# Kernel tuning notes

Measured on AMD Instinct MI355X. Metric: run time of the kernel, lower is better.

Reference implementation:

```python
import jax, jax.numpy as jnp
import numpy as np

B, S, E, O, LAYERS = 256, 28, 256, 256, 3


def setup_inputs() -> dict:
    key = jax.random.key(0)
    ks = jax.random.split(key, 20)
    sc = 0.05
    inp = {
        "centers": jax.random.normal(ks[0], (B, S, 3), jnp.float32),
        "object_embedding": jax.random.normal(ks[1], (B, S, E), jnp.float32),
        "counts": jax.random.randint(ks[2], (B,), 1, S + 1),
        # linear_relation_object: 3 -> E
        "Wr": jax.random.normal(ks[3], (E, 3), jnp.float32) * sc,
        "br": jnp.zeros((E,), jnp.float32),
        # LSTM (PyTorch gate order i,f,g,o)
        "W_ih": jax.random.normal(ks[4], (4 * O, E), jnp.float32) * sc,
        "W_hh": jax.random.normal(ks[5], (4 * O, O), jnp.float32) * sc,
        "b_ih": jnp.zeros((4 * O,), jnp.float32),
        "b_hh": jnp.zeros((4 * O,), jnp.float32),
        # gr: 3E -> O
        "Wgr": jax.random.normal(ks[6], (O, 3 * E), jnp.float32) * sc,
        "bgr": jnp.zeros((O,), jnp.float32),
        # bezier control: O -> O, plus scalar alpha
        "Wbc": jax.random.normal(ks[7], (O, O), jnp.float32) * sc,
        "bbc": jnp.zeros((O,), jnp.float32),
        "alpha": jnp.asarray(0.5, jnp.float32),
        # esa: E -> O
        "Wesa": jax.random.normal(ks[8], (O, E), jnp.float32) * sc,
        "besa": jnp.zeros((O,), jnp.float32),
        # gaussian heads: O -> 3
        "Wmu": jax.random.normal(ks[9], (3, O), jnp.float32) * sc,
        "bmu": jnp.zeros((3,), jnp.float32),
        "Wlv": jax.random.normal(ks[10], (3, O), jnp.float32) * sc,
        "blv": jnp.zeros((3,), jnp.float32),
    }
    return inp


def _lstm(x, W_ih, W_hh, b_ih, b_hh):
    # x: [B,S,E] -> hs: [B,S,O], zero initial state, PyTorch gate order i,f,g,o
    Bdim = x.shape[0]
    Odim = W_hh.shape[1]
    b = b_ih + b_hh

    def step(carry, xt):
        h, c = carry
        z = xt @ W_ih.T + h @ W_hh.T + b  # [B,4O]
        i, f, g, o = jnp.split(z, 4, axis=-1)
        c = jax.nn.sigmoid(f) * c + jax.nn.sigmoid(i) * jnp.tanh(g)
        h = jax.nn.sigmoid(o) * jnp.tanh(c)
        return (h, c), h

    h0 = jnp.zeros((Bdim, Odim), x.dtype)
    _, hs = jax.lax.scan(step, (h0, h0), jnp.swapaxes(x, 0, 1))
    return jnp.swapaxes(hs, 0, 1)


def reference(centers, object_embedding, counts, Wr, br, W_ih, W_hh, b_ih, b_hh,
              Wgr, bgr, Wbc, bbc, alpha, Wesa, besa, Wmu, bmu, Wlv, blv):
    # masks from per-scene object counts (padding replication of the torch loops)
    idx = jnp.arange(S)
    obj_mask = (idx[None, :] < counts[:, None]).astype(jnp.float32)[..., None]  # [B,S,1]
    rel_mask = (obj_mask[:, :, None, :] * obj_mask[:, None, :, :])              # [B,S,S,1]

    centers_p = centers * obj_mask                     # padded centers are zero
    relation = centers_p[:, :, None, :] - centers_p[:, None, :, :]  # [B,S,S,3]
    rlf = relation @ Wr.T + br                         # [B,S,S,E]

    olf = object_embedding * obj_mask                  # [B,S,E]
    t = jax.nn.sigmoid(alpha)

    for _ in range(LAYERS):
        new_olf = _lstm(olf, W_ih, W_hh, b_ih, b_hh) * obj_mask
        rep_i = jnp.broadcast_to(olf[:, :, None, :], (olf.shape[0], S, S, olf.shape[-1]))
        rep_j = jnp.broadcast_to(olf[:, None, :, :], (olf.shape[0], S, S, olf.shape[-1]))
        cat = jnp.concatenate([rep_i, rep_j, rlf], axis=-1)   # [B,S,S,3E]
        rlf_lin = cat @ Wgr.T + bgr                           # [B,S,S,O]
        cp = rlf_lin @ Wbc.T + bbc
        bez = ((1 - t) ** 2 + t ** 2) * rlf_lin + 2 * (1 - t) * t * cp
        rlf = jnp.tanh(bez) * rel_mask
        olf = new_olf

    rlf = rlf @ Wesa.T + besa                                  # [B,S,S,O]
    # base attention: softmax over dim=1 (explicit max-subtract as in source)
    base_attn = jax.nn.softmax(rlf - jnp.max(rlf, axis=1, keepdims=True), axis=1)
    # gaussian attention (eval mode: eps = 0 -> samples = mus)
    mus = rlf @ Wmu.T + bmu                                    # [B,S,S,3]
    _logvars = rlf @ Wlv.T + blv                               # computed, unused at eval
    gscores = jnp.mean(mus, axis=-1, keepdims=True)            # [B,S,S,1]
    gattn = jax.nn.softmax(gscores, axis=1)
    attn = 0.5 * base_attn + 0.5 * gattn                       # broadcast over O
    rel_out = jnp.sum(attn * rlf, axis=-2) * obj_mask          # [B,S,O]
    return rel_out
```

## Files before the change

### kernel.cpp

```cpp
#include <hip/hip_runtime.h>


typedef __attribute__((ext_vector_type(8))) short short8;
typedef __attribute__((ext_vector_type(4))) float f32x4;

__device__ __forceinline__ float b2f(unsigned short u){
  union { unsigned int i; float f; } v; v.i = ((unsigned int)u) << 16; return v.f;
}
__device__ __forceinline__ float u2f(unsigned int u){
  union { unsigned int i; float f; } v; v.i = u; return v.f;
}
__device__ __forceinline__ unsigned short f2b(float f){
  union { float f; unsigned int i; } v; v.f = f;
  return (unsigned short)((v.i + 0x8000u) >> 16);
}
__device__ __forceinline__ unsigned int pk2(float lo, float hi){
  union { float f; unsigned int i; } a, b; a.f = lo; b.f = hi;
  return __builtin_amdgcn_perm(b.i + 0x8000u, a.i + 0x8000u, 0x07060302u);
}
__device__ __forceinline__ float sigm(float x){ return 1.f/(1.f+__expf(-x)); }
__device__ __forceinline__ float tanh_f(float x){ float e = __expf(2.f*x); return 1.f - 2.f/(e+1.f); }
__device__ __forceinline__ int xsw(int row, int n){
  int c = n >> 3;
  int pc = (c & 24) | ((c ^ row) & 7);
  return row*256 + pc*8 + (n & 7);
}

#define MFMA16(a,b,c) __builtin_amdgcn_mfma_f32_16x16x32_bf16((a),(b),(c),0,0,0)

__global__ __launch_bounds__(256) void k_reprep(const float* __restrict__ Wih,
                                                const float* __restrict__ Whh,
                                                const float* __restrict__ Wgr,
                                                const float* __restrict__ Wbc,
                                                const float* __restrict__ Wesa,
                                                const float* __restrict__ Wmu,
                                                unsigned short* __restrict__ wcv,
                                                float* __restrict__ wmean,
                                                const float* __restrict__ emb,
                                                const int* __restrict__ counts,
                                                unsigned short* __restrict__ olf,
                                                float* __restrict__ out){
  if (blockIdx.x >= 3329){
    int bs = blockIdx.x - 3329;
    int b = bs / 28; int s = bs - b*28;
    int e = threadIdx.x;
    olf[(size_t)bs*256 + e] = (s < counts[b]) ? f2b(emb[(size_t)bs*256 + e]) : (unsigned short)0;
    out[(size_t)bs*256 + e] = 0.f;
    return;
  }
  int i = blockIdx.x*256 + threadIdx.x;
  if (i >= 851968){
    int o = i - 851968;
    if (o < 256) wmean[o] = (Wmu[o] + Wmu[256+o] + Wmu[512+o]) * (1.f/3.f);
    return;
  }
  const float* s; int segbase, N, stride, off, local;
  if      (i < 262144){ s=Wih;  segbase=0;      N=1024; stride=256; off=0;   local=i; }
  else if (i < 524288){ s=Whh;  segbase=262144; N=1024; stride=256; off=0;   local=i-262144; }
  else if (i < 589824){ s=Wgr;  segbase=524288; N=256;  stride=768; off=0;   local=i-524288; }
  else if (i < 655360){ s=Wgr;  segbase=589824; N=256;  stride=768; off=256; local=i-589824; }
  else if (i < 720896){ s=Wgr;  segbase=655360; N=256;  stride=768; off=512; local=i-655360; }
  else if (i < 786432){ s=Wbc;  segbase=720896; N=256;  stride=256; off=0;   local=i-720896; }
  else                { s=Wesa; segbase=786432; N=256;  stride=256; off=0;   local=i-786432; }
  int n = local >> 8, k = local & 255;
  wcv[segbase + (((k >> 3)*N + n) << 3) + (k & 7)] = f2b(s[n*stride + off + k]);
}

__global__ __launch_bounds__(256) void k_xgemm(const unsigned short* __restrict__ olf,
                                               const unsigned short* __restrict__ Wih,
                                               unsigned short* __restrict__ zx){
  const int tid = threadIdx.x;
  const int wid = tid >> 6, lane = tid & 63, col = lane & 15, quad = lane >> 4;
  const int m0 = (blockIdx.x >> 1)*64 + wid*16;
  const int nt0 = (blockIdx.x & 1)*32;
  short8 af[8];
  #pragma unroll
  for (int kt=0; kt<8; ++kt)
    af[kt] = *(const short8*)&olf[(size_t)(m0 + col)*256 + kt*32 + quad*8];
  #pragma unroll 4
  for (int nt=nt0; nt<nt0+32; ++nt){
    int n = nt*16 + col;
    f32x4 acc = (f32x4){0.f,0.f,0.f,0.f};
    #pragma unroll
    for (int kt=0; kt<8; ++kt){
      short8 bf = *(const short8*)&Wih[((((kt*4 + quad) << 10) + n) << 3)];
      acc = MFMA16(bf, af[kt], acc);
    }
    *(uint2*)&zx[(size_t)(m0 + col)*1024 + nt*16 + quad*4] =
        make_uint2(pk2(acc[0],acc[1]), pk2(acc[2],acc[3]));
  }
}

__global__ __launch_bounds__(1024) void k_recat(const unsigned short* __restrict__ zx,
                                                const unsigned short* __restrict__ Whh,
                                                const float* __restrict__ bih,
                                                const float* __restrict__ bhh,
                                                const int* __restrict__ counts,
                                                unsigned short* __restrict__ olf_out,
                                                const unsigned short* __restrict__ olf_at,
                                                const unsigned short* __restrict__ Wgri,
                                                const unsigned short* __restrict__ Wgrj,
                                                const float* __restrict__ bgr,
                                                unsigned short* __restrict__ At_out){
  __shared__ unsigned short Ab[2][16*264];
  const int tid = threadIdx.x;
  const int wv = tid >> 6, lane = tid & 63, col = lane & 15, quad = lane >> 4;

  if (blockIdx.x >= 16){
    const int m0 = (blockIdx.x - 16)*256 + wv*16;
    short8 af[8];
    #pragma unroll
    for (int kt=0; kt<8; ++kt)
      af[kt] = *(const short8*)&olf_at[(size_t)(m0 + col)*256 + kt*32 + quad*8];
    #pragma unroll 4
    for (int nt=0; nt<32; ++nt){
      const unsigned short* wb = (nt < 16) ? Wgri : Wgrj;
      int nb = (nt < 16) ? 0 : 256;
      int nn = (nt & 15)*16 + col;
      f32x4 bg4 = (nt < 16) ? *(const f32x4*)&bgr[(nt & 15)*16 + quad*4]
                            : (f32x4){0.f,0.f,0.f,0.f};
      f32x4 acc = (f32x4){0.f,0.f,0.f,0.f};
      #pragma unroll
      for (int kt=0; kt<8; ++kt){
        short8 bf = *(const short8*)&wb[((((kt*4 + quad) << 8) + nn) << 3)];
        acc = MFMA16(bf, af[kt], acc);
      }
      acc += bg4;
      *(uint2*)&At_out[(size_t)(m0 + col)*512 + nb + (nt & 15)*16 + quad*4] =
          make_uint2(pk2(acc[0],acc[1]), pk2(acc[2],acc[3]));
    }
    return;
  }
  const int sc0 = blockIdx.x * 16;
  const int u = wv*16 + col;
  float bz[4];
  #pragma unroll
  for (int g=0; g<4; ++g) bz[g] = bih[g*256+u] + bhh[g*256+u];
  int cnt4[4];
  #pragma unroll
  for (int r=0; r<4; ++r) cnt4[r] = counts[sc0 + quad*4 + r];

  float cst[4];
  #pragma unroll
  for (int r=0; r<4; ++r) cst[r] = 0.f;
  for (int i=tid; i<16*264; i+=1024) Ab[0][i] = 0;
  __syncthreads();

  for (int t=0; t<28; ++t){
    const int cur = t & 1, nxt = cur ^ 1;
    float zxv[4][4];
    #pragma unroll
    for (int g=0; g<4; ++g){
      #pragma unroll
      for (int r=0; r<4; ++r)
        zxv[g][r] = b2f(zx[((size_t)(sc0 + quad*4 + r)*28 + t)*1024 + g*256 + u]);
    }
    f32x4 acc[4];
    #pragma unroll
    for (int g=0; g<4; ++g) acc[g] = (f32x4){0.f,0.f,0.f,0.f};
    #pragma unroll
    for (int kt=0; kt<8; ++kt){
      short8 a = *(const short8*)&Ab[cur][col*264 + kt*32 + quad*8];
      #pragma unroll
      for (int g=0; g<4; ++g){
        short8 bf = *(const short8*)&Whh[((((kt*4 + quad) << 10) + g*256 + u) << 3)];
        acc[g] = MFMA16(a, bf, acc[g]);
      }
    }
    #pragma unroll
    for (int r=0; r<4; ++r){
      int s = quad*4 + r;
      float zi = acc[0][r] + zxv[0][r] + bz[0];
      float zf = acc[1][r] + zxv[1][r] + bz[1];
      float zg = acc[2][r] + zxv[2][r] + bz[2];
      float zo = acc[3][r] + zxv[3][r] + bz[3];
      float cc = sigm(zf)*cst[r] + sigm(zi)*tanh_f(zg);
      cst[r] = cc;
      float hh = sigm(zo)*tanh_f(cc);
      unsigned short hb = f2b(hh);
      Ab[nxt][s*264 + u] = hb;
      olf_out[((size_t)(sc0+s)*28 + t)*256 + u] = (t < cnt4[r]) ? hb : (unsigned short)0;
    }
    __syncthreads();
  }
}

__global__ __launch_bounds__(256) void k_aterm(const unsigned short* __restrict__ olf,
                                               const unsigned short* __restrict__ Wgri,
                                               const unsigned short* __restrict__ Wgrj,
                                               const float* __restrict__ bgr,
                                               unsigned short* __restrict__ Aout){
  const int tid = threadIdx.x;
  const int wid = tid >> 6, lane = tid & 63, col = lane & 15, quad = lane >> 4;
  const int m0 = blockIdx.x*64 + wid*16;
  short8 af[8];
  #pragma unroll
  for (int kt=0; kt<8; ++kt)
    af[kt] = *(const short8*)&olf[(size_t)(m0 + col)*256 + kt*32 + quad*8];
  #pragma unroll 4
  for (int nt=0; nt<32; ++nt){
    const unsigned short* wb = (nt < 16) ? Wgri : Wgrj;
    int nb = (nt < 16) ? 0 : 256;
    int nn = (nt & 15)*16 + col;
    f32x4 bg4 = (nt < 16) ? *(const f32x4*)&bgr[(nt & 15)*16 + quad*4]
                          : (f32x4){0.f,0.f,0.f,0.f};
    f32x4 acc = (f32x4){0.f,0.f,0.f,0.f};
    #pragma unroll
    for (int kt=0; kt<8; ++kt){
      short8 bf = *(const short8*)&wb[((((kt*4 + quad) << 8) + nn) << 3)];
      acc = MFMA16(bf, af[kt], acc);
    }
    acc += bg4;
    *(uint2*)&Aout[(size_t)(m0 + col)*512 + nb + (nt & 15)*16 + quad*4] =
        make_uint2(pk2(acc[0],acc[1]), pk2(acc[2],acc[3]));
  }
}

#define GEMM_TILE64(SRC, WPTR)                                                      \
  {                                                                                 \
    _Pragma("unroll")                                                               \
    for (int rf=0; rf<4; ++rf){ Ya[rf][0]=(f32x4){0.f,0.f,0.f,0.f};                 \
                                Ya[rf][1]=(f32x4){0.f,0.f,0.f,0.f}; }               \
    _Pragma("unroll 1")                                                             \
    for (int kc=0; kc<4; ++kc){                                                     \
      short8 av[2][4], bv[2][2];                                                    \
      _Pragma("unroll")                                                             \
      for (int u=0; u<2; ++u){                                                      \
        int kt = kc*2 + u;                                                          \
        _Pragma("unroll")                                                           \
        for (int rf=0; rf<4; ++rf)                                                  \
          av[u][rf] = *(const short8*)&(SRC)[(Abase[rf] + kc*64) ^ (u*32)];         \
        bv[u][0] = *(const short8*)&(WPTR)[Bbase + kt*8192];                        \
        bv[u][1] = *(const short8*)&(WPTR)[Bbase + kt*8192 + 128];                  \
      }                                                                             \
      __builtin_amdgcn_s_setprio(1);                                                \
      _Pragma("unroll")                                                             \
      for (int u=0; u<2; ++u){                                                      \
        _Pragma("unroll")                                                           \
        for (int rf=0; rf<4; ++rf){                                                 \
          Ya[rf][0] = MFMA16(bv[u][0], av[u][rf], Ya[rf][0]);                       \
          Ya[rf][1] = MFMA16(bv[u][1], av[u][rf], Ya[rf][1]);                       \
        }                                                                           \
      }                                                                             \
      __builtin_amdgcn_s_setprio(0);                                                \
    }                                                                               \
  }

__global__ __launch_bounds__(512, 4) void k_mega(
    const float* __restrict__ centers, const int* __restrict__ counts,
    const float* __restrict__ Wr, const float* __restrict__ br,
    const unsigned short* __restrict__ Wgrr, const float* __restrict__ bgr,
    const unsigned short* __restrict__ Wbc, const float* __restrict__ bbc,
    const float* __restrict__ alpha,
    const unsigned short* __restrict__ Wesa, const float* __restrict__ besa,
    const float* __restrict__ wmean, const float* __restrict__ bmu,
    const unsigned short* __restrict__ Aterm, float* __restrict__ out){
  __shared__ unsigned short Xa[64*256];
  __shared__ unsigned short Yb[64*256];
  float* hrSBp = (float*)&Xa[56*256];
  float* gsbp  = (float*)&Xa[60*256];
  float* hrSGp = (float*)&Xa[60*256+128];
  const int tid = threadIdx.x;
  const int wv = tid >> 6;
  const int lane = tid & 63, col = lane & 15, quad = lane >> 4;
  const int xcd = blockIdx.x & 7, idx = blockIdx.x >> 3;
  const int b = xcd*32 + idx/14, jt = idx - (idx/14)*14;
  const int cb = counts[b];
  const int nbase = wv*32;

  float av_ = alpha[0];
  float tv = sigm(av_);
  float c1 = (1.f-tv)*(1.f-tv) + tv*tv;
  float c2 = 2.f*tv*(1.f-tv);

  float pv[4];
  const unsigned short* apI[4];
  const unsigned short* apJ[4];
  #pragma unroll
  for (int mt=0; mt<4; ++mt){
    int m = mt*16 + col;
    int i = m >> 1;
    int pi = (i < 27) ? i : 27;
    int pj = jt*2 + (m & 1);
    pv[mt] = (m < 56 && i < cb && pj < cb) ? 1.f : 0.f;
    apI[mt] = Aterm + (size_t)(b*28 + pi)*512 + nbase + quad*4;
    apJ[mt] = Aterm + (size_t)(b*28 + pj)*512 + 256 + nbase + quad*4;
  }
  int Abase[4];
  #pragma unroll
  for (int rf=0; rf<4; ++rf){
    int row = rf*16 + col;
    Abase[rf] = row*256 + ((quad ^ (row & 3)) | (row & 4))*8;
  }
  const int Bbase = (quad*256 + nbase + col)*8;
  int woff[4][2];
  f32x4 cbb[2], bev[2];
  #pragma unroll
  for (int nt2=0; nt2<2; ++nt2){
    int n0 = nbase + nt2*16 + quad*4;
    cbb[nt2] = (*(const f32x4*)&bbc[n0]) * c2;
    bev[nt2] = *(const f32x4*)&besa[n0];
    #pragma unroll
    for (int mt=0; mt<4; ++mt)
      woff[mt][nt2] = xsw(mt*16 + col, n0);
  }

  {
    int m = tid >> 3, sub = tid & 7;
    int i = m >> 1, j = jt*2 + (m & 1);
    bool valid = (m < 56);
    float mi = (valid && i < cb) ? 1.f : 0.f;
    float mj = (valid && j < cb) ? 1.f : 0.f;
    float vm = valid ? 1.f : 0.f;
    const float* ci = centers + (b*28 + (valid ? i : 0))*3;
    const float* cj = centers + (b*28 + j)*3;
    float dx = mi*ci[0] - mj*cj[0];
    float dy = mi*ci[1] - mj*cj[1];
    float dz = mi*ci[2] - mj*cj[2];
    #pragma unroll
    for (int c8=0; c8<4; ++c8){
      int e0 = sub*32 + c8*8;
      f32x4 w0 = *(const f32x4*)&Wr[e0*3 +  0];
      f32x4 w1 = *(const f32x4*)&Wr[e0*3 +  4];
      f32x4 w2 = *(const f32x4*)&Wr[e0*3 +  8];
      f32x4 w3 = *(const f32x4*)&Wr[e0*3 + 12];
      f32x4 w4 = *(const f32x4*)&Wr[e0*3 + 16];
      f32x4 w5 = *(const f32x4*)&Wr[e0*3 + 20];
      f32x4 b0 = *(const f32x4*)&br[e0];
      f32x4 b1 = *(const f32x4*)&br[e0+4];
      b0 *= vm; b1 *= vm;
      float v0 = dx*w0[0] + dy*w0[1] + dz*w0[2] + b0[0];
      float v1 = dx*w0[3] + dy*w1[0] + dz*w1[1] + b0[1];
      float v2 = dx*w1[2] + dy*w1[3] + dz*w2[0] + b0[2];
      float v3 = dx*w2[1] + dy*w2[2] + dz*w2[3] + b0[3];
      float v4 = dx*w3[0] + dy*w3[1] + dz*w3[2] + b1[0];
      float v5 = dx*w3[3] + dy*w4[0] + dz*w4[1] + b1[1];
      float v6 = dx*w4[2] + dy*w4[3] + dz*w5[0] + b1[2];
      float v7 = dx*w5[1] + dy*w5[2] + dz*w5[3] + b1[3];
      uint4 pw;
      pw.x = pk2(v0,v1); pw.y = pk2(v2,v3); pw.z = pk2(v4,v5); pw.w = pk2(v6,v7);
      *(uint4*)&Xa[xsw(m, e0)] = pw;
    }
  }
  __syncthreads();

  f32x4 Ya[4][2];
  #pragma unroll 1
  for (int l=0; l<3; ++l){
    uint2 rAi[4][2], rAj[4][2];
    #pragma unroll
    for (int mt=0; mt<4; ++mt){
      rAi[mt][0] = *(const uint2*)&apI[mt][0];
      rAi[mt][1] = *(const uint2*)&apI[mt][16];
      rAj[mt][0] = *(const uint2*)&apJ[mt][0];
      rAj[mt][1] = *(const uint2*)&apJ[mt][16];
      apI[mt] += 7168*512; apJ[mt] += 7168*512;
    }
    GEMM_TILE64(Xa, Wgrr);
    #pragma unroll
    for (int nt2=0; nt2<2; ++nt2){
      #pragma unroll
      for (int mt=0; mt<4; ++mt){
        uint2 wi = rAi[mt][nt2], wj = rAj[mt][nt2];
        f32x4 ai, aj;
        ai[0] = u2f(wi.x << 16); ai[1] = u2f(wi.x & 0xffff0000u);
        ai[2] = u2f(wi.y << 16); ai[3] = u2f(wi.y & 0xffff0000u);
        aj[0] = u2f(wj.x << 16); aj[1] = u2f(wj.x & 0xffff0000u);
        aj[2] = u2f(wj.y << 16); aj[3] = u2f(wj.y & 0xffff0000u);
        f32x4 v = Ya[mt][nt2] + ai + aj;
        *(uint2*)&Yb[woff[mt][nt2]] = make_uint2(pk2(v[0],v[1]), pk2(v[2],v[3]));
      }
    }
    __syncthreads();
    GEMM_TILE64(Yb, Wbc);
    #pragma unroll
    for (int nt2=0; nt2<2; ++nt2){
      #pragma unroll
      for (int mt=0; mt<4; ++mt){
        uint2 w = *(const uint2*)&Yb[woff[mt][nt2]];
        f32x4 rl;
        rl[0] = u2f(w.x << 16); rl[1] = u2f(w.x & 0xffff0000u);
        rl[2] = u2f(w.y << 16); rl[3] = u2f(w.y & 0xffff0000u);
        f32x4 bez = Ya[mt][nt2]*c2 + cbb[nt2];
        bez = rl*c1 + bez;
        float x0 = tanh_f(bez[0]) * pv[mt];
        float x1 = tanh_f(bez[1]) * pv[mt];
        float x2 = tanh_f(bez[2]) * pv[mt];
        float x3 = tanh_f(bez[3]) * pv[mt];
        *(uint2*)&Xa[woff[mt][nt2]] = make_uint2(pk2(x0,x1), pk2(x2,x3));
      }
    }
    __syncthreads();
  }
  GEMM_TILE64(Xa, Wesa);
  __syncthreads();
  f32x4 sbp[2] = {(f32x4){0.f,0.f,0.f,0.f}, (f32x4){0.f,0.f,0.f,0.f}};
  const float m3f = (col < 8) ? 1.f : 0.f;
  #pragma unroll
  for (int nt2=0; nt2<2; ++nt2){
    #pragma unroll
    for (int mt=0; mt<4; ++mt){
      f32x4 v = Ya[mt][nt2] + bev[nt2];
      *(uint2*)&Yb[woff[mt][nt2]] = make_uint2(pk2(v[0],v[1]), pk2(v[2],v[3]));
      f32x4 e;
      e[0] = __expf(v[0]); e[1] = __expf(v[1]);
      e[2] = __expf(v[2]); e[3] = __expf(v[3]);
      *(uint2*)&Xa[woff[mt][nt2]] = make_uint2(pk2(e[0],e[1]), pk2(e[2],e[3]));
      f32x4 wsum = e;
      if (mt == 3) wsum *= m3f;
      sbp[nt2] += wsum;
    }
  }
  f32x4 hr[2];
  #pragma unroll
  for (int nt2=0; nt2<2; ++nt2){
    #pragma unroll
    for (int r=0; r<4; ++r){
      float s = sbp[nt2][r];
      s += __shfl_xor(s, 2, 64);
      s += __shfl_xor(s, 4, 64);
      s += __shfl_xor(s, 8, 64);
      hr[nt2][r] = 0.5f / s;
    }
  }
  __syncthreads();
  {
    int m = tid >> 3, sub = tid & 7;
    if (m < 56){
      float s = 0.f;
      #pragma unroll
      for (int c8=0; c8<4; ++c8){
        int e0 = sub*32 + c8*8;
        uint4 u = *(const uint4*)&Yb[xsw(m, e0)];
        f32x4 wm0 = *(const f32x4*)&wmean[e0];
        f32x4 wm1 = *(const f32x4*)&wmean[e0+4];
        s += u2f(u.x << 16)*wm0[0] + u2f(u.x & 0xffff0000u)*wm0[1]
           + u2f(u.y << 16)*wm0[2] + u2f(u.y & 0xffff0000u)*wm0[3]
           + u2f(u.z << 16)*wm1[0] + u2f(u.z & 0xffff0000u)*wm1[1]
           + u2f(u.w << 16)*wm1[2] + u2f(u.w & 0xffff0000u)*wm1[3];
      }
      s += __shfl_xor(s, 1, 64);
      s += __shfl_xor(s, 2, 64);
      s += __shfl_xor(s, 4, 64);
      if (sub == 0)
        gsbp[m] = __expf(s + (bmu[0] + bmu[1] + bmu[2])*(1.f/3.f));
    }
  }
  if (col < 2){
    #pragma unroll
    for (int nt2=0; nt2<2; ++nt2){
      #pragma unroll
      for (int r=0; r<4; ++r)
        hrSBp[col*256 + nbase + nt2*16 + quad*4 + r] = hr[nt2][r];
    }
  }
  __syncthreads();
  if (tid < 64){
    float g = (tid < 56) ? gsbp[tid] : 0.f;
    g += __shfl_xor(g, 2, 64);
    g += __shfl_xor(g, 4, 64);
    g += __shfl_xor(g, 8, 64);
    g += __shfl_xor(g, 16, 64);
    g += __shfl_xor(g, 32, 64);
    if (tid < 2) hrSGp[tid] = 0.5f / g;
  }
  __syncthreads();
  for (int it = tid; it < 7168; it += 512){
    int i = it >> 8, o = it & 255;
    if (i < cb){
      float s = 0.f;
      #pragma unroll
      for (int jc=0; jc<2; ++jc){
        int row = i*2 + jc;
        int off = xsw(row, o);
        float v = b2f(Yb[off]);
        float E = b2f(Xa[off]);
        float a = E*hrSBp[jc*256+o] + gsbp[row]*hrSGp[jc];
        s += a * v;
      }
      atomicAdd(&out[((size_t)b*28 + i)*256 + o], s);
    }
  }
}

extern "C" void kernel_launch(void* const* d_in, const int* in_sizes, int n_in,
                              void* d_out, int out_size, void* d_ws, size_t ws_size,
                              hipStream_t stream){
  const float* centers = (const float*)d_in[0];
  const float* emb     = (const float*)d_in[1];
  const int*   counts  = (const int*)d_in[2];
  const float* Wr      = (const float*)d_in[3];
  const float* br      = (const float*)d_in[4];
  const float* Wih     = (const float*)d_in[5];
  const float* Whh     = (const float*)d_in[6];
  const float* bih     = (const float*)d_in[7];
  const float* bhh     = (const float*)d_in[8];
  const float* Wgr     = (const float*)d_in[9];
  const float* bgr     = (const float*)d_in[10];
  const float* Wbc     = (const float*)d_in[11];
  const float* bbc     = (const float*)d_in[12];
  const float* alpha   = (const float*)d_in[13];
  const float* Wesa    = (const float*)d_in[14];
  const float* besa    = (const float*)d_in[15];
  const float* Wmu     = (const float*)d_in[16];
  const float* bmu     = (const float*)d_in[17];

  unsigned short* olf   = (unsigned short*)d_ws;
  unsigned short* At    = (unsigned short*)((char*)d_ws + 11010048);
  unsigned short* zx    = (unsigned short*)((char*)d_ws + 33030144);
  unsigned short* wcv   = (unsigned short*)((char*)d_ws + 47710208);
  float*          wmean = (float*)((char*)d_ws + 49414144);
  unsigned short* cWih  = wcv;
  unsigned short* cWhh  = wcv + 262144;
  unsigned short* cWgri = wcv + 524288;
  unsigned short* cWgrj = wcv + 589824;
  unsigned short* cWgrr = wcv + 655360;
  unsigned short* cWbc  = wcv + 720896;
  unsigned short* cWesa = wcv + 786432;
  float* outp = (float*)d_out;

  unsigned short* olf1 = olf + (size_t)7168*256;
  unsigned short* olf2 = olf + (size_t)2*7168*256;
  unsigned short* At1  = At  + (size_t)7168*512;
  unsigned short* At2  = At  + (size_t)2*7168*512;

  hipLaunchKernelGGL(k_reprep, dim3(10497), dim3(256), 0, stream,
                     Wih, Whh, Wgr, Wbc, Wesa, Wmu, wcv, wmean,
                     emb, counts, olf, outp);
  hipLaunchKernelGGL(k_xgemm, dim3(224), dim3(256), 0, stream, olf, cWih, zx);
  hipLaunchKernelGGL(k_recat, dim3(44), dim3(1024), 0, stream,
                     zx, cWhh, bih, bhh, counts, olf1, olf, cWgri, cWgrj, bgr, At);
  hipLaunchKernelGGL(k_xgemm, dim3(224), dim3(256), 0, stream, olf1, cWih, zx);
  hipLaunchKernelGGL(k_recat, dim3(44), dim3(1024), 0, stream,
                     zx, cWhh, bih, bhh, counts, olf2, olf1, cWgri, cWgrj, bgr, At1);
  hipLaunchKernelGGL(k_aterm, dim3(112), dim3(256), 0, stream, olf2, cWgri, cWgrj, bgr, At2);
  hipLaunchKernelGGL(k_mega,  dim3(3584), dim3(512), 0, stream,
                     centers, counts, Wr, br, cWgrr, bgr, cWbc, bbc, alpha,
                     cWesa, besa, wmean, bmu, At, outp);
}
```

Measured before the change: 1.176 ms.

## Move At-term GEMM into x-GEMM launch and prefetch next-step zx in recurrence

The per-layer At projection (olf times Wgr i/j) moves out of the recurrent LSTM kernel and into the input-projection GEMM launch as an extra 112 blocks. The recurrence kernel now launches only 16 large blocks. The recurrence also prefetches the next timestep's zx values into registers before the MMA work, so global load latency is hidden behind compute on the serial critical path. The cost is more register pressure in the recurrent kernel and a larger GEMM grid.

Result: slower. 1.269 ms (+7.9%).

```diff
diff --git a/kernel.cpp b/kernel.cpp
--- a/kernel.cpp
+++ b/kernel.cpp
@@ -66,52 +66,21 @@
   wcv[segbase + (((k >> 3)*N + n) << 3) + (k & 7)] = f2b(s[n*stride + off + k]);
 }
 
-__global__ __launch_bounds__(256) void k_xgemm(const unsigned short* __restrict__ olf,
-                                               const unsigned short* __restrict__ Wih,
-                                               unsigned short* __restrict__ zx){
+__global__ __launch_bounds__(256) void k_xgemm_at(const unsigned short* __restrict__ olf,
+                                                  const unsigned short* __restrict__ Wih,
+                                                  unsigned short* __restrict__ zx,
+                                                  const unsigned short* __restrict__ Wgri,
+                                                  const unsigned short* __restrict__ Wgrj,
+                                                  const float* __restrict__ bgr,
+                                                  unsigned short* __restrict__ At_out){
   const int tid = threadIdx.x;
   const int wid = tid >> 6, lane = tid & 63, col = lane & 15, quad = lane >> 4;
-  const int m0 = (blockIdx.x >> 1)*64 + wid*16;
-  const int nt0 = (blockIdx.x & 1)*32;
-  short8 af[8];
-  #pragma unroll
-  for (int kt=0; kt<8; ++kt)
-    af[kt] = *(const short8*)&olf[(size_t)(m0 + col)*256 + kt*32 + quad*8];
-  #pragma unroll 4
-  for (int nt=nt0; nt<nt0+32; ++nt){
-    int n = nt*16 + col;
-    f32x4 acc = (f32x4){0.f,0.f,0.f,0.f};
-    #pragma unroll
-    for (int kt=0; kt<8; ++kt){
-      short8 bf = *(const short8*)&Wih[((((kt*4 + quad) << 10) + n) << 3)];
-      acc = MFMA16(bf, af[kt], acc);
-    }
-    *(uint2*)&zx[(size_t)(m0 + col)*1024 + nt*16 + quad*4] =
-        make_uint2(pk2(acc[0],acc[1]), pk2(acc[2],acc[3]));
-  }
-}
-
-__global__ __launch_bounds__(1024) void k_recat(const unsigned short* __restrict__ zx,
-                                                const unsigned short* __restrict__ Whh,
-                                                const float* __restrict__ bih,
-                                                const float* __restrict__ bhh,
-                                                const int* __restrict__ counts,
-                                                unsigned short* __restrict__ olf_out,
-                                                const unsigned short* __restrict__ olf_at,
-                                                const unsigned short* __restrict__ Wgri,
-                                                const unsigned short* __restrict__ Wgrj,
-                                                const float* __restrict__ bgr,
-                                                unsigned short* __restrict__ At_out){
-  __shared__ unsigned short Ab[2][16*264];
-  const int tid = threadIdx.x;
-  const int wv = tid >> 6, lane = tid & 63, col = lane & 15, quad = lane >> 4;
-
-  if (blockIdx.x >= 16){
-    const int m0 = (blockIdx.x - 16)*256 + wv*16;
+  if (blockIdx.x >= 224){
+    const int m0 = (blockIdx.x - 224)*64 + wid*16;
     short8 af[8];
     #pragma unroll
     for (int kt=0; kt<8; ++kt)
-      af[kt] = *(const short8*)&olf_at[(size_t)(m0 + col)*256 + kt*32 + quad*8];
+      af[kt] = *(const short8*)&olf[(size_t)(m0 + col)*256 + kt*32 + quad*8];
     #pragma unroll 4
     for (int nt=0; nt<32; ++nt){
       const unsigned short* wb = (nt < 16) ? Wgri : Wgrj;
@@ -131,6 +100,35 @@
     }
     return;
   }
+  const int m0 = (blockIdx.x >> 1)*64 + wid*16;
+  const int nt0 = (blockIdx.x & 1)*32;
+  short8 af[8];
+  #pragma unroll
+  for (int kt=0; kt<8; ++kt)
+    af[kt] = *(const short8*)&olf[(size_t)(m0 + col)*256 + kt*32 + quad*8];
+  #pragma unroll 4
+  for (int nt=nt0; nt<nt0+32; ++nt){
+    int n = nt*16 + col;
+    f32x4 acc = (f32x4){0.f,0.f,0.f,0.f};
+    #pragma unroll
+    for (int kt=0; kt<8; ++kt){
+      short8 bf = *(const short8*)&Wih[((((kt*4 + quad) << 10) + n) << 3)];
+      acc = MFMA16(bf, af[kt], acc);
+    }
+    *(uint2*)&zx[(size_t)(m0 + col)*1024 + nt*16 + quad*4] =
+        make_uint2(pk2(acc[0],acc[1]), pk2(acc[2],acc[3]));
+  }
+}
+
+__global__ __launch_bounds__(1024) void k_rec(const unsigned short* __restrict__ zx,
+                                              const unsigned short* __restrict__ Whh,
+                                              const float* __restrict__ bih,
+                                              const float* __restrict__ bhh,
+                                              const int* __restrict__ counts,
+                                              unsigned short* __restrict__ olf_out){
+  __shared__ unsigned short Ab[2][16*264];
+  const int tid = threadIdx.x;
+  const int wv = tid >> 6, lane = tid & 63, col = lane & 15, quad = lane >> 4;
   const int sc0 = blockIdx.x * 16;
   const int u = wv*16 + col;
   float bz[4];
@@ -144,16 +142,24 @@
   #pragma unroll
   for (int r=0; r<4; ++r) cst[r] = 0.f;
   for (int i=tid; i<16*264; i+=1024) Ab[0][i] = 0;
+
+  float zxv[4][4], zxn[4][4];
+  #pragma unroll
+  for (int g=0; g<4; ++g){
+    #pragma unroll
+    for (int r=0; r<4; ++r)
+      zxv[g][r] = b2f(zx[((size_t)(sc0 + quad*4 + r)*28 + 0)*1024 + g*256 + u]);
+  }
   __syncthreads();
 
   for (int t=0; t<28; ++t){
     const int cur = t & 1, nxt = cur ^ 1;
-    float zxv[4][4];
+    const int tn = (t < 27) ? t + 1 : 27;
     #pragma unroll
     for (int g=0; g<4; ++g){
       #pragma unroll
       for (int r=0; r<4; ++r)
-        zxv[g][r] = b2f(zx[((size_t)(sc0 + quad*4 + r)*28 + t)*1024 + g*256 + u]);
+        zxn[g][r] = b2f(zx[((size_t)(sc0 + quad*4 + r)*28 + tn)*1024 + g*256 + u]);
     }
     f32x4 acc[4];
     #pragma unroll
@@ -182,6 +188,11 @@
       olf_out[((size_t)(sc0+s)*28 + t)*256 + u] = (t < cnt4[r]) ? hb : (unsigned short)0;
     }
     __syncthreads();
+    #pragma unroll
+    for (int g=0; g<4; ++g){
+      #pragma unroll
+      for (int r=0; r<4; ++r) zxv[g][r] = zxn[g][r];
+    }
   }
 }
 
@@ -527,12 +538,14 @@
   hipLaunchKernelGGL(k_reprep, dim3(10497), dim3(256), 0, stream,
                      Wih, Whh, Wgr, Wbc, Wesa, Wmu, wcv, wmean,
                      emb, counts, olf, outp);
-  hipLaunchKernelGGL(k_xgemm, dim3(224), dim3(256), 0, stream, olf, cWih, zx);
-  hipLaunchKernelGGL(k_recat, dim3(44), dim3(1024), 0, stream,
-                     zx, cWhh, bih, bhh, counts, olf1, olf, cWgri, cWgrj, bgr, At);
-  hipLaunchKernelGGL(k_xgemm, dim3(224), dim3(256), 0, stream, olf1, cWih, zx);
-  hipLaunchKernelGGL(k_recat, dim3(44), dim3(1024), 0, stream,
-                     zx, cWhh, bih, bhh, counts, olf2, olf1, cWgri, cWgrj, bgr, At1);
+  hipLaunchKernelGGL(k_xgemm_at, dim3(336), dim3(256), 0, stream,
+                     olf, cWih, zx, cWgri, cWgrj, bgr, At);
+  hipLaunchKernelGGL(k_rec, dim3(16), dim3(1024), 0, stream,
+                     zx, cWhh, bih, bhh, counts, olf1);
+  hipLaunchKernelGGL(k_xgemm_at, dim3(336), dim3(256), 0, stream,
+                     olf1, cWih, zx, cWgri, cWgrj, bgr, At1);
+  hipLaunchKernelGGL(k_rec, dim3(16), dim3(1024), 0, stream,
+                     zx, cWhh, bih, bhh, counts, olf2);
   hipLaunchKernelGGL(k_aterm, dim3(112), dim3(256), 0, stream, olf2, cWgri, cWgrj, bgr, At2);
   hipLaunchKernelGGL(k_mega,  dim3(3584), dim3(512), 0, stream,
                      centers, counts, Wr, br, cWgrr, bgr, cWbc, bbc, alpha,
```
